# Kernel optimization log

Measured on AMD Instinct MI355X. Metric: run time of the kernel, lower is better.

## Reference

```python
import jax, jax.numpy as jnp
import numpy as np

DN3D = ('NCDHW', 'OIDHW', 'NCDHW')

def conv_t3d(x, w, stride):
    # PyTorch ConvTranspose3d with padding=0: w is (C_in, C_out, k1,k2,k3).
    # Equivalent dilated conv: flip spatial dims, swap in/out channels,
    # lhs_dilation=stride, padding k-1 on each side.
    wf = jnp.flip(w, axis=(2, 3, 4)).transpose(1, 0, 2, 3, 4)  # (O, I, k, k, k)
    pad = [(k - 1, k - 1) for k in w.shape[2:]]
    dn = jax.lax.conv_dimension_numbers(x.shape, wf.shape, DN3D)
    return jax.lax.conv_general_dilated(x, wf, (1, 1, 1), pad,
                                        lhs_dilation=stride, dimension_numbers=dn)

def conv3d(x, w, stride, pad):
    dn = jax.lax.conv_dimension_numbers(x.shape, w.shape, DN3D)
    return jax.lax.conv_general_dilated(x, w, stride, [(pad, pad)] * 3,
                                        dimension_numbers=dn)

def setup_inputs() -> dict:
    key = jax.random.key(0)
    ks = jax.random.split(key, 7)
    out_ch, emb, p = 4, 256, 8
    B, T, D = 2, 8, 4  # batch, 4th spatial dim, coarse grid (input_size//patch_size)
    s = 0.05
    return {
        'x':  jax.random.normal(ks[0], (B, T, out_ch * emb, D, D, D), jnp.float32),
        'w1': jax.random.normal(ks[1], (out_ch * emb, out_ch * 2, p // 2, p // 2, p // 2), jnp.float32) * s,
        'b1': jax.random.normal(ks[2], (out_ch * 2,), jnp.float32) * s,
        'w2': jax.random.normal(ks[3], (out_ch * 2, out_ch * 2, 4, 4, 4), jnp.float32) * s,
        'b2': jax.random.normal(ks[4], (out_ch * 2,), jnp.float32) * s,
        'w3': jax.random.normal(ks[5], (out_ch, out_ch * 2, 4, 4, 4), jnp.float32) * s,
        'b3': jax.random.normal(ks[6], (out_ch,), jnp.float32) * s,
    }

def reference(x, w1, b1, w2, b2, w3, b3):
    # x: (B, D4, C_in, D1, D2, D3). All 4D kernels are size/stride 1 along D4,
    # so fold D4 into the batch and run 3D (de)convs.
    B, T, C, D, _, _ = x.shape
    h = x.reshape(B * T, C, D, D, D)
    bcast = lambda b: b[None, :, None, None, None]
    h = jnp.tanh(conv_t3d(h, w1, (4, 4, 4)) + bcast(b1))   # -> (BT, 8, 16,16,16)
    h = jnp.tanh(conv_t3d(h, w2, (4, 4, 4)) + bcast(b2))   # -> (BT, 8, 64,64,64)
    h = conv3d(h, w3, (2, 2, 2), 1) + bcast(b3)             # -> (BT, 4, 32,32,32)
    out = h.reshape(B, T, *h.shape[1:])                     # (B, D4, C, 32,32,32)
    return jnp.moveaxis(out, 1, -1)                         # (B, C, 32,32,32, D4)
```

## Files before the change

### kernel.cpp

```cpp
#include <hip/hip_runtime.h>
#include <cstdint>

typedef _Float16 f16x8 __attribute__((ext_vector_type(8)));
typedef float f32x4 __attribute__((ext_vector_type(4)));
typedef _Float16 half2_t __attribute__((ext_vector_type(2)));

__device__ __forceinline__ unsigned pkh2(float a, float b) {
  return __builtin_bit_cast(unsigned, __builtin_amdgcn_cvt_pkrtz(a, b));
}
__device__ __forceinline__ float fast_tanh(float x) {
  float e = __builtin_amdgcn_exp2f(x * 2.885390081777927f);
  return 1.0f - 2.0f * __builtin_amdgcn_rcpf(e + 1.0f);
}

#if __has_builtin(__builtin_amdgcn_fdot2)
__device__ __forceinline__ float dot2h(unsigned a, unsigned b, float c) {
  return __builtin_amdgcn_fdot2(__builtin_bit_cast(half2_t, a),
                                __builtin_bit_cast(half2_t, b), c, false);
}
#else
__device__ __forceinline__ float dot2h(unsigned a, unsigned b, float c) {
  half2_t av = __builtin_bit_cast(half2_t, a);
  half2_t bv = __builtin_bit_cast(half2_t, b);
  c = fmaf((float)av.x, (float)bv.x, c);
  c = fmaf((float)av.y, (float)bv.y, c);
  return c;
}
#endif

template <int ITERS>
__global__ __launch_bounds__(256, 4) void k_stage1(const float* __restrict__ x,
                                                   const float* __restrict__ w1,
                                                   const float* __restrict__ w3,
                                                   float* __restrict__ part,
                                                   unsigned* __restrict__ wtab) {
  constexpr int NS = 32 / ITERS;
  constexpr int KSB = (NS == 8) ? 3 : (NS == 4) ? 2 : (NS == 2) ? 1 : 0;
  __shared__ __align__(16) char lds_raw[64 * 65 * 4];
  unsigned short* As = (unsigned short*)lds_raw;
  unsigned short* Bs = (unsigned short*)(lds_raw + 5120);
  float* Cs = (float*)lds_raw;

  const int tid = threadIdx.x;
  if (blockIdx.x == 0) {
    int l = tid << 2;
#pragma unroll
    for (int j = 0; j < 4; ++j) {
      int d = l + j;
      int slot = d & 3, chU = (d >> 2) & 1, kh = (d >> 3) & 3,
          kd = (d >> 5) & 3, cio = d >> 7;
      int co = (chU << 1) + (slot & 1);
      int kwb = (slot >> 1) << 1;
      int base = ((co << 3) + cio) * 64 + (kd << 4) + (kh << 2) + kwb;
      wtab[d] = pkh2(w3[base], w3[base + 1]);
    }
  }

  const int ks = blockIdx.x & (NS - 1);
  const int bt = (blockIdx.x >> KSB) & 15;
  const int co = blockIdx.x >> (KSB + 4);
  const int w = tid >> 6, lane = tid & 63, lm = lane & 15, q = lane >> 4;
  const int rrow = tid & 63, kgr = tid >> 6;

  f32x4 acc[4];
#pragma unroll
  for (int i = 0; i < 4; ++i) acc[i] = (f32x4){0.f, 0.f, 0.f, 0.f};

  const float* gA = x + (bt << 16) + ((size_t)(ks * ITERS * 32) << 6);
  const float* gB = w1 + (co << 6) + (size_t)(ks * ITERS * 32) * 512;

  float va[2][8], vb[2][8];
#define S1_LOAD(buf, it)                            \
  {                                                 \
    const int kb = (it) * 32 + (kgr << 3);          \
    _Pragma("unroll") for (int j = 0; j < 8; ++j) { \
      va[buf][j] = gA[((kb + j) << 6) | rrow];      \
      vb[buf][j] = gB[(kb + j) * 512 + rrow];       \
    }                                               \
  }
  S1_LOAD(0, 0);
#pragma unroll
  for (int it = 0; it < ITERS; ++it) {
    const int cur = it & 1;
    if (it + 1 < ITERS) S1_LOAD(cur ^ 1, it + 1);
    uint4 pa, pb;
    pa.x = pkh2(va[cur][0], va[cur][1]);
    pa.y = pkh2(va[cur][2], va[cur][3]);
    pa.z = pkh2(va[cur][4], va[cur][5]);
    pa.w = pkh2(va[cur][6], va[cur][7]);
    pb.x = pkh2(vb[cur][0], vb[cur][1]);
    pb.y = pkh2(vb[cur][2], vb[cur][3]);
    pb.z = pkh2(vb[cur][4], vb[cur][5]);
    pb.w = pkh2(vb[cur][6], vb[cur][7]);
    *(uint4*)&As[rrow * 40 + (kgr << 3)] = pa;
    *(uint4*)&Bs[rrow * 40 + (kgr << 3)] = pb;
    __syncthreads();
    f16x8 a = *(const f16x8*)&As[((w << 4) + lm) * 40 + (q << 3)];
#pragma unroll
    for (int nf = 0; nf < 4; ++nf) {
      f16x8 b = *(const f16x8*)&Bs[((nf << 4) + lm) * 40 + (q << 3)];
      acc[nf] = __builtin_amdgcn_mfma_f32_16x16x32_f16(a, b, acc[nf], 0, 0, 0);
    }
    __syncthreads();
  }
#undef S1_LOAD
#pragma unroll
  for (int nf = 0; nf < 4; ++nf)
#pragma unroll
    for (int r = 0; r < 4; ++r) {
      int m = (w << 4) + (q << 2) + r;
      int n = (nf << 4) + lm;
      Cs[m * 65 + n] = acc[nf][r];
    }
  __syncthreads();
  float* dst = part + (((size_t)(((ks << 4) + bt) << 3) + co) << 12);
#pragma unroll
  for (int j = 0; j < 4; ++j) {
    int pos = (tid << 2) + (j << 10);
    int z = pos >> 8, y = (pos >> 4) & 15, xx = pos & 15;
    int m = ((z >> 2) << 4) + ((y >> 2) << 2) + (xx >> 2);
    int n = ((z & 3) << 4) + ((y & 3) << 2);
    float4 v;
    v.x = Cs[m * 65 + n + 0];
    v.y = Cs[m * 65 + n + 1];
    v.z = Cs[m * 65 + n + 2];
    v.w = Cs[m * 65 + n + 3];
    *(float4*)&dst[pos] = v;
  }
}

__global__ __launch_bounds__(512) void k_stage23(
    const float* __restrict__ part, const float* __restrict__ w2,
    const float* __restrict__ b2, const float* __restrict__ b3,
    const float* __restrict__ b1, const unsigned* __restrict__ wtab,
    float* __restrict__ out, int nsplit) {
  __shared__ __align__(16) unsigned win_d[2][18 * 34 * 12];
  __shared__ __align__(16) unsigned h1p[6 * 240];
  __shared__ __align__(16) unsigned w2p[8 * 320];

  const int tid = threadIdx.x;
  const int bid = blockIdx.x;
  const int bt = bid >> 5;
  const int tile = bid & 31;
  const int tz = tile >> 3, ty = (tile >> 2) & 1, tx = tile & 3;
  const int Z0 = tz << 3, Y0 = ty << 4, X0 = tx << 3;
  const int Qz0 = (Z0 << 1) - 1, Qy0 = (Y0 << 1) - 1, Qx0 = (X0 << 1) - 1;
  const int Uz0 = (tz << 2) - 1, Uy0 = (ty << 3) - 1, Ux0 = (tx << 2) - 1;

  for (int l = tid; l < 2880; l += 512) {
    int ci = l / 360;
    int sp = l - ci * 360;
    int ux = sp % 6;
    int t1 = sp / 6;
    int uy = t1 % 10;
    int uz = t1 / 10;
    int gz = Uz0 + uz, gy = Uy0 + uy, gx = Ux0 + ux;
    float v = 0.f;
    if ((unsigned)gz < 16u && (unsigned)gy < 16u && (unsigned)gx < 16u) {
      const float* p =
          part + (((size_t)(bt << 3) + ci) << 12) + (gz << 8) + (gy << 4) + gx;
      float s = b1[ci];
      for (int sg = 0; sg < nsplit; ++sg) s += p[(size_t)sg << 19];
      v = fast_tanh(s);
    }
    ((_Float16*)h1p)[uz * 480 + uy * 48 + (ux << 3) + ci] = (_Float16)v;
  }
  for (int l = tid; l < 2048; l += 512) {
    int j = l & 3, kx = (l >> 2) & 3, kzy = (l >> 4) & 15, cio = l >> 8;
    int kpos = (kzy << 2) + kx;
    float w0 = w2[(((j << 1) << 3) + cio) * 64 + kpos];
    float w1v = w2[((((j << 1) + 1) << 3) + cio) * 64 + kpos];
    w2p[cio * 320 + kzy * 20 + (kx << 2) + j] = pkh2(w0, w1v);
  }
  for (int u = tid; u < 1224; u += 512) {
    int wz = u / 68;
    int rem = u - wz * 68;
    int wy = rem >> 1;
    int half = rem & 1;
    int qz = Qz0 + wz, qy = Qy0 + wy;
    if ((unsigned)qz < 64u && (unsigned)qy < 64u) continue;
    uint4 zz;
    zz.x = zz.y = zz.z = zz.w = 0u;
#pragma unroll
    for (int bsel = 0; bsel < 2; ++bsel) {
      unsigned* wrow = win_d[bsel] + (wz * 34 + wy) * 12;
      if (half == 0) {
        *(uint4*)wrow = zz;
      } else {
        *(uint4*)(wrow + 4) = zz;
        wrow[8] = 0u;
      }
    }
  }
  __syncthreads();

  float acc[2][4];
#pragma unroll
  for (int a = 0; a < 2; ++a)
#pragma unroll
    for (int i = 0; i < 4; ++i) acc[a][i] = 0.f;

  const int xh = tid & 1, yq = (tid >> 1) & 15, zq = (tid >> 5) & 7;
  const int chS = __builtin_amdgcn_readfirstlane(tid >> 8);

  for (int cio = 0; cio < 8; ++cio) {
    unsigned* wbuf = win_d[cio & 1];
    const float b2c = b2[cio];
    for (int u = tid; u < 1224; u += 512) {
      int wz = u / 68;
      int rem = u - wz * 68;
      int wy = rem >> 1;
      int half = rem & 1;
      int qz = Qz0 + wz, qy = Qy0 + wy;
      if (!((unsigned)qz < 64u && (unsigned)qy < 64u)) continue;
      unsigned* wrow = wbuf + (wz * 34 + wy) * 12;
      int kz = qz & 3, ky = qy & 3;
      int uzp = (qz >> 2) - Uz0, uyp = (qy >> 2) - Uy0;
      const unsigned* w2b = w2p + cio * 320 + ((kz << 2) + ky) * 20;
      uint4 wv[4];
#pragma unroll
      for (int kx = 0; kx < 4; ++kx) wv[kx] = *(const uint4*)(w2b + (kx << 2));
      const unsigned* h1b = h1p + uzp * 240 + uyp * 24;
#define DOT8(hc, kx)                                            \
  dot2h((hc).w, wv[kx].w,                                       \
        dot2h((hc).z, wv[kx].z,                                 \
              dot2h((hc).y, wv[kx].y, dot2h((hc).x, wv[kx].x, b2c))))
      if (half == 0) {
        uint4 h0 = *(const uint4*)(h1b);
        uint4 h1c = *(const uint4*)(h1b + 4);
        uint4 h2c = *(const uint4*)(h1b + 8);
        float vals[8];
        vals[0] = (Qx0 >= 0) ? fast_tanh(DOT8(h0, 3)) : 0.f;
#pragma unroll
        for (int kx = 0; kx < 4; ++kx) vals[1 + kx] = fast_tanh(DOT8(h1c, kx));
#pragma unroll
        for (int kx = 0; kx < 3; ++kx) vals[5 + kx] = fast_tanh(DOT8(h2c, kx));
        uint4 s0;
        s0.x = pkh2(vals[0], vals[1]);
        s0.y = pkh2(vals[2], vals[3]);
        s0.z = pkh2(vals[4], vals[5]);
        s0.w = pkh2(vals[6], vals[7]);
        *(uint4*)wrow = s0;
      } else {
        uint4 h2c = *(const uint4*)(h1b + 8);
        uint4 h3 = *(const uint4*)(h1b + 12);
        uint4 h4 = *(const uint4*)(h1b + 16);
        uint4 h5 = *(const uint4*)(h1b + 20);
        float vals[10];
        vals[0] = fast_tanh(DOT8(h2c, 3));
#pragma unroll
        for (int kx = 0; kx < 4; ++kx) vals[1 + kx] = fast_tanh(DOT8(h3, kx));
#pragma unroll
        for (int kx = 0; kx < 4; ++kx) vals[5 + kx] = fast_tanh(DOT8(h4, kx));
        vals[9] = (Qx0 + 17 < 64) ? fast_tanh(DOT8(h5, 0)) : 0.f;
        uint4 s1;
        s1.x = pkh2(vals[0], vals[1]);
        s1.y = pkh2(vals[2], vals[3]);
        s1.z = pkh2(vals[4], vals[5]);
        s1.w = pkh2(vals[6], vals[7]);
        *(uint4*)(wrow + 4) = s1;
        wrow[8] = pkh2(vals[8], vals[9]);
      }
#undef DOT8
    }
    __syncthreads();
#pragma unroll
    for (int kd = 0; kd < 4; ++kd) {
      int wz = (zq << 1) + kd;
#pragma unroll
      for (int kh = 0; kh < 4; ++kh) {
        int wy = (yq << 1) + kh;
        const unsigned* rowp = wbuf + (wz * 34 + wy) * 12 + (xh << 2);
        uint4 rv = *(const uint4*)rowp;
        unsigned r4 = rowp[4];
        unsigned r[5] = {rv.x, rv.y, rv.z, rv.w, r4};
        const uint4 wv =
            *(const uint4*)&wtab[((((cio << 4) + (kd << 2) + kh) << 1) + chS)
                                 << 2];
        unsigned wA[2] = {wv.x, wv.y};
        unsigned wB[2] = {wv.z, wv.w};
#pragma unroll
        for (int cc = 0; cc < 2; ++cc) {
#pragma unroll
          for (int i = 0; i < 4; ++i) {
            float a0 = dot2h(r[i], wA[cc], acc[cc][i]);
            acc[cc][i] = dot2h(r[i + 1], wB[cc], a0);
          }
        }
      }
    }
  }
  const int ch = tid >> 8;
  const int b = bt >> 3, t8 = bt & 7;
  const int z = Z0 + zq;
  const int y = Y0 + yq;
#pragma unroll
  for (int cc = 0; cc < 2; ++cc) {
    int c4 = (ch << 1) + cc;
    float bias = b3[c4];
#pragma unroll
    for (int i = 0; i < 4; ++i) {
      int xx = X0 + (xh << 2) + i;
      out[(((((b << 2) + c4) * 32 + z) * 32 + y) * 32 + xx) << 3 | t8] =
          acc[cc][i] + bias;
    }
  }
}

extern "C" void kernel_launch(void* const* d_in, const int* in_sizes, int n_in,
                              void* d_out, int out_size, void* d_ws,
                              size_t ws_size, hipStream_t stream) {
  (void)in_sizes; (void)n_in; (void)out_size;
  const float* x = (const float*)d_in[0];
  const float* w1 = (const float*)d_in[1];
  const float* b1 = (const float*)d_in[2];
  const float* w2 = (const float*)d_in[3];
  const float* b2 = (const float*)d_in[4];
  const float* w3 = (const float*)d_in[5];
  const float* b3 = (const float*)d_in[6];
  float* out = (float*)d_out;
  float* part = (float*)d_ws;

  const size_t plane = (size_t)16 * 8 * 4096;
  int nsplit = 1;
  if (ws_size >= 8 * plane * 4 + 4096)
    nsplit = 8;
  else if (ws_size >= 4 * plane * 4 + 4096)
    nsplit = 4;
  else if (ws_size >= 2 * plane * 4 + 4096)
    nsplit = 2;
  unsigned* wtab = (unsigned*)(part + (size_t)nsplit * plane);

  switch (nsplit) {
    case 8:
      k_stage1<4><<<dim3(1024), dim3(256), 0, stream>>>(x, w1, w3, part, wtab);
      break;
    case 4:
      k_stage1<8><<<dim3(512), dim3(256), 0, stream>>>(x, w1, w3, part, wtab);
      break;
    case 2:
      k_stage1<16><<<dim3(256), dim3(256), 0, stream>>>(x, w1, w3, part, wtab);
      break;
    default:
      k_stage1<32><<<dim3(128), dim3(256), 0, stream>>>(x, w1, w3, part, wtab);
      break;
  }
  k_stage23<<<dim3(512), dim3(512), 0, stream>>>(part, w2, b2, b3, b1, wtab,
                                                 out, nsplit);
}
```

Baseline: 154.8 us.

## Template stage23 on split count, prefetch partial sums, hoist fill indexing

Stage 2/3 becomes a template on the split count, so the partial-sum reduction unrolls fully. The partial-sum loads are issued early into registers and only reduced after the weight packing and halo zeroing, so load latency overlaps other setup work. Per-thread fill-loop index math is precomputed once outside the channel loop. The block-to-tile mapping is also transposed, and the maximum split drops from 8 to 4, giving fewer stage-1 blocks with more K each and fewer partials to reduce. The cost is higher register pressure from holding up to 24 prefetched values per thread.

```diff
diff --git a/kernel.cpp b/kernel.cpp
--- a/kernel.cpp
+++ b/kernel.cpp
@@ -129,42 +129,54 @@
   }
 }
 
+template <int NSPLIT>
 __global__ __launch_bounds__(512) void k_stage23(
     const float* __restrict__ part, const float* __restrict__ w2,
     const float* __restrict__ b2, const float* __restrict__ b3,
     const float* __restrict__ b1, const unsigned* __restrict__ wtab,
-    float* __restrict__ out, int nsplit) {
+    float* __restrict__ out) {
   __shared__ __align__(16) unsigned win_d[2][18 * 34 * 12];
   __shared__ __align__(16) unsigned h1p[6 * 240];
   __shared__ __align__(16) unsigned w2p[8 * 320];
 
   const int tid = threadIdx.x;
   const int bid = blockIdx.x;
-  const int bt = bid >> 5;
-  const int tile = bid & 31;
+  const int bt = bid & 15;
+  const int tile = bid >> 4;
   const int tz = tile >> 3, ty = (tile >> 2) & 1, tx = tile & 3;
   const int Z0 = tz << 3, Y0 = ty << 4, X0 = tx << 3;
   const int Qz0 = (Z0 << 1) - 1, Qy0 = (Y0 << 1) - 1, Qx0 = (X0 << 1) - 1;
   const int Uz0 = (tz << 2) - 1, Uy0 = (ty << 3) - 1, Ux0 = (tx << 2) - 1;
 
-  for (int l = tid; l < 2880; l += 512) {
-    int ci = l / 360;
-    int sp = l - ci * 360;
+  float sv[6][NSPLIT];
+  float b1v[6];
+  int dsto[6];
+  bool inb[6];
+#pragma unroll
+  for (int k = 0; k < 6; ++k) {
+    int l = tid + (k << 9);
+    bool vld = l < 2880;
+    int ll = vld ? l : 0;
+    int ci = ll / 360;
+    int sp = ll - ci * 360;
     int ux = sp % 6;
     int t1 = sp / 6;
     int uy = t1 % 10;
     int uz = t1 / 10;
     int gz = Uz0 + uz, gy = Uy0 + uy, gx = Ux0 + ux;
-    float v = 0.f;
-    if ((unsigned)gz < 16u && (unsigned)gy < 16u && (unsigned)gx < 16u) {
+    inb[k] = vld && (unsigned)gz < 16u && (unsigned)gy < 16u &&
+             (unsigned)gx < 16u;
+    dsto[k] = vld ? (uz * 480 + uy * 48 + (ux << 3) + ci) : -1;
+    b1v[k] = 0.f;
+    if (inb[k]) {
+      b1v[k] = b1[ci];
       const float* p =
           part + (((size_t)(bt << 3) + ci) << 12) + (gz << 8) + (gy << 4) + gx;
-      float s = b1[ci];
-      for (int sg = 0; sg < nsplit; ++sg) s += p[(size_t)sg << 19];
-      v = fast_tanh(s);
-    }
-    ((_Float16*)h1p)[uz * 480 + uy * 48 + (ux << 3) + ci] = (_Float16)v;
-  }
+#pragma unroll
+      for (int sg = 0; sg < NSPLIT; ++sg) sv[k][sg] = p[(size_t)sg << 19];
+    }
+  }
+
   for (int l = tid; l < 2048; l += 512) {
     int j = l & 3, kx = (l >> 2) & 3, kzy = (l >> 4) & 15, cio = l >> 8;
     int kpos = (kzy << 2) + kx;
@@ -192,6 +204,41 @@
       }
     }
   }
+
+#pragma unroll
+  for (int k = 0; k < 6; ++k) {
+    if (dsto[k] < 0) continue;
+    float v = 0.f;
+    if (inb[k]) {
+      float s = b1v[k];
+#pragma unroll
+      for (int sg = 0; sg < NSPLIT; ++sg) s += sv[k][sg];
+      v = fast_tanh(s);
+    }
+    ((_Float16*)h1p)[dsto[k]] = (_Float16)v;
+  }
+
+  int fu_row[3], fu_h1[3], fu_w2[3], fu_half[3];
+  bool fu_act[3];
+#pragma unroll
+  for (int k = 0; k < 3; ++k) {
+    int u = tid + (k << 9);
+    bool act = u < 1224;
+    int uu = act ? u : 0;
+    int wz = uu / 68;
+    int rem = uu - wz * 68;
+    int wy = rem >> 1, half = rem & 1;
+    int qz = Qz0 + wz, qy = Qy0 + wy;
+    fu_act[k] = act && (unsigned)qz < 64u && (unsigned)qy < 64u;
+    fu_row[k] = (wz * 34 + wy) * 12;
+    int kz = qz & 3, ky = qy & 3;
+    fu_w2[k] = ((kz << 2) + ky) * 20;
+    int uzp = (qz >> 2) - Uz0, uyp = (qy >> 2) - Uy0;
+    fu_h1[k] = uzp * 240 + uyp * 24;
+    fu_half[k] = half;
+  }
+  const bool gLo = (Qx0 >= 0), gHi = (Qx0 + 17 < 64);
+
   __syncthreads();
 
   float acc[2][4];
@@ -206,31 +253,25 @@
   for (int cio = 0; cio < 8; ++cio) {
     unsigned* wbuf = win_d[cio & 1];
     const float b2c = b2[cio];
-    for (int u = tid; u < 1224; u += 512) {
-      int wz = u / 68;
-      int rem = u - wz * 68;
-      int wy = rem >> 1;
-      int half = rem & 1;
-      int qz = Qz0 + wz, qy = Qy0 + wy;
-      if (!((unsigned)qz < 64u && (unsigned)qy < 64u)) continue;
-      unsigned* wrow = wbuf + (wz * 34 + wy) * 12;
-      int kz = qz & 3, ky = qy & 3;
-      int uzp = (qz >> 2) - Uz0, uyp = (qy >> 2) - Uy0;
-      const unsigned* w2b = w2p + cio * 320 + ((kz << 2) + ky) * 20;
+#pragma unroll
+    for (int k = 0; k < 3; ++k) {
+      if (!fu_act[k]) continue;
+      unsigned* wrow = wbuf + fu_row[k];
+      const unsigned* w2b = w2p + cio * 320 + fu_w2[k];
       uint4 wv[4];
 #pragma unroll
       for (int kx = 0; kx < 4; ++kx) wv[kx] = *(const uint4*)(w2b + (kx << 2));
-      const unsigned* h1b = h1p + uzp * 240 + uyp * 24;
+      const unsigned* h1b = h1p + fu_h1[k];
 #define DOT8(hc, kx)                                            \
   dot2h((hc).w, wv[kx].w,                                       \
         dot2h((hc).z, wv[kx].z,                                 \
               dot2h((hc).y, wv[kx].y, dot2h((hc).x, wv[kx].x, b2c))))
-      if (half == 0) {
+      if (fu_half[k] == 0) {
         uint4 h0 = *(const uint4*)(h1b);
         uint4 h1c = *(const uint4*)(h1b + 4);
         uint4 h2c = *(const uint4*)(h1b + 8);
         float vals[8];
-        vals[0] = (Qx0 >= 0) ? fast_tanh(DOT8(h0, 3)) : 0.f;
+        vals[0] = gLo ? fast_tanh(DOT8(h0, 3)) : 0.f;
 #pragma unroll
         for (int kx = 0; kx < 4; ++kx) vals[1 + kx] = fast_tanh(DOT8(h1c, kx));
 #pragma unroll
@@ -252,7 +293,7 @@
         for (int kx = 0; kx < 4; ++kx) vals[1 + kx] = fast_tanh(DOT8(h3, kx));
 #pragma unroll
         for (int kx = 0; kx < 4; ++kx) vals[5 + kx] = fast_tanh(DOT8(h4, kx));
-        vals[9] = (Qx0 + 17 < 64) ? fast_tanh(DOT8(h5, 0)) : 0.f;
+        vals[9] = gHi ? fast_tanh(DOT8(h5, 0)) : 0.f;
         uint4 s1;
         s1.x = pkh2(vals[0], vals[1]);
         s1.y = pkh2(vals[2], vals[3]);
@@ -323,28 +364,27 @@
 
   const size_t plane = (size_t)16 * 8 * 4096;
   int nsplit = 1;
-  if (ws_size >= 8 * plane * 4 + 4096)
-    nsplit = 8;
-  else if (ws_size >= 4 * plane * 4 + 4096)
+  if (ws_size >= 4 * plane * 4 + 4096)
     nsplit = 4;
   else if (ws_size >= 2 * plane * 4 + 4096)
     nsplit = 2;
   unsigned* wtab = (unsigned*)(part + (size_t)nsplit * plane);
 
   switch (nsplit) {
-    case 8:
-      k_stage1<4><<<dim3(1024), dim3(256), 0, stream>>>(x, w1, w3, part, wtab);
-      break;
     case 4:
       k_stage1<8><<<dim3(512), dim3(256), 0, stream>>>(x, w1, w3, part, wtab);
+      k_stage23<4><<<dim3(512), dim3(512), 0, stream>>>(part, w2, b2, b3, b1,
+                                                        wtab, out);
       break;
     case 2:
       k_stage1<16><<<dim3(256), dim3(256), 0, stream>>>(x, w1, w3, part, wtab);
+      k_stage23<2><<<dim3(512), dim3(512), 0, stream>>>(part, w2, b2, b3, b1,
+                                                        wtab, out);
       break;
     default:
       k_stage1<32><<<dim3(128), dim3(256), 0, stream>>>(x, w1, w3, part, wtab);
+      k_stage23<1><<<dim3(512), dim3(512), 0, stream>>>(part, w2, b2, b3, b1,
+                                                        wtab, out);
       break;
   }
-  k_stage23<<<dim3(512), dim3(512), 0, stream>>>(part, w2, b2, b3, b1, wtab,
-                                                 out, nsplit);
-}
+}
```

Measured after the change: 140.7 us. 1.1x faster.
